# Kernel optimization log

Measured on AMD Instinct MI355X. Metric: run time of the kernel, lower is better.

The kernel has to match this reference:

```python
import jax, jax.numpy as jnp
import numpy as np

U = 128  # linear_units

def setup_inputs() -> dict:
    key = jax.random.key(0)
    k1, k2, k3, k4, k5, k6 = jax.random.split(key, 6)
    B, S, D = 16, 2048, 128
    x = jax.random.normal(k1, (B, S, D), dtype=jnp.float32)
    t = jax.random.uniform(k2, (B, S), dtype=jnp.float32)
    # glorot_uniform inits
    lim_qk = np.sqrt(6.0 / (D + U)).astype(np.float32)
    Wq = jax.random.uniform(k3, (D, U), minval=-lim_qk, maxval=lim_qk, dtype=jnp.float32)
    Wk = jax.random.uniform(k4, (D, U), minval=-lim_qk, maxval=lim_qk, dtype=jnp.float32)
    lim_s = np.sqrt(6.0 / (1 + S)).astype(np.float32)
    theta = jax.random.uniform(k5, (1, S), minval=-lim_s, maxval=lim_s, dtype=jnp.float32)
    mu = jax.random.uniform(k6, (1, S), minval=-lim_s, maxval=lim_s, dtype=jnp.float32)
    return {"x": x, "t": t, "Wq": Wq, "Wk": Wk, "theta": theta, "mu": mu}

def reference(x, t, Wq, Wk, theta, mu):
    # x: (B,S,D), t: (B,S), theta/mu: (1,S)
    scale = jnp.sqrt(jnp.asarray(U, dtype=x.dtype))
    q = x @ Wq                                   # (B,S,U)
    k = x @ Wk                                   # (B,S,U)
    scores = jnp.einsum('biu,bju->bij', q, k) / scale  # (B,S,S)
    alphas = jax.nn.softmax(scores, axis=-1)
    gn = jnp.einsum('bij,bjd->bid', alphas, x)   # weighted sum == alphas @ x, (B,S,D)
    time_fact = jax.nn.sigmoid(theta - mu * t)   # (B,S)
    v = jnp.sum(gn * time_fact[:, :, None], axis=1)  # (B,D)
    return v
```

## Files before the change

### kernel.cpp

```cpp
#include <hip/hip_runtime.h>
#include <hip/hip_bf16.h>

#define SS 2048
#define DD 128
#define BB 16
#define LDST 136
#define SCT 268

typedef short bf16x8 __attribute__((ext_vector_type(8)));
typedef float f32x4 __attribute__((ext_vector_type(4)));
typedef unsigned short ushort_t;

__device__ __forceinline__ unsigned short f2bf(float f) {
  union { float f; unsigned u; } v; v.f = f;
  unsigned r = v.u + 0x7fffu + ((v.u >> 16) & 1u);
  return (unsigned short)(r >> 16);
}
__device__ __forceinline__ float fexp2(float x) { return __builtin_amdgcn_exp2f(x); }


__global__ __launch_bounds__(256) void wprep(
    const float* __restrict__ Wq, const float* __restrict__ Wk,
    ushort_t* __restrict__ wt_g) {
  int idx = blockIdx.x * 256 + threadIdx.x;
  int r = idx & 16383, uu = r >> 7, d = r & 127;
  if (idx < 16384)
    wt_g[uu * 128 + d] = f2bf(Wq[d * 128 + uu] * 0.1275174346f);
  else
    wt_g[(uu + 128) * 128 + d] = f2bf(Wk[d * 128 + uu]);
}

__global__ __launch_bounds__(256, 2) void qk_gemm(
    const float* __restrict__ x, const ushort_t* __restrict__ wt_g,
    uint4* __restrict__ qF, uint4* __restrict__ kF) {
  __shared__ ushort_t xs[64 * LDST];
  __shared__ ushort_t sc[64 * SCT];
  const int tid = threadIdx.x, wave = tid >> 6, lane = tid & 63;
  const int lq = lane & 15, quad = lane >> 4;
  const int m0 = blockIdx.x * 64;

#pragma unroll
  for (int i = 0; i < 8; ++i) {
    int idx = i * 256 + tid;
    int row = idx >> 5, c4 = (idx & 31) * 4;
    const float4 v = *(const float4*)(x + (size_t)(m0 + row) * DD + c4);
    ushort4 h;
    h.x = f2bf(v.x); h.y = f2bf(v.y); h.z = f2bf(v.z); h.w = f2bf(v.w);
    *(ushort4*)(&xs[row * LDST + c4]) = h;
  }
  bf16x8 wf[4][4];
#pragma unroll
  for (int nt = 0; nt < 4; ++nt)
#pragma unroll
    for (int ks = 0; ks < 4; ++ks)
      wf[nt][ks] = *(const bf16x8*)(wt_g + (wave * 64 + nt * 16 + lq) * 128 + ks * 32 + quad * 8);
  __syncthreads();

  f32x4 acc[4][4];
#pragma unroll
  for (int mt = 0; mt < 4; ++mt)
#pragma unroll
    for (int nt = 0; nt < 4; ++nt) acc[mt][nt] = (f32x4){0.f, 0.f, 0.f, 0.f};
#pragma unroll
  for (int mt = 0; mt < 4; ++mt) {
    bf16x8 af[4];
#pragma unroll
    for (int ks = 0; ks < 4; ++ks)
      af[ks] = *(const bf16x8*)(&xs[(mt * 16 + lq) * LDST + ks * 32 + quad * 8]);
#pragma unroll
    for (int nt = 0; nt < 4; ++nt)
#pragma unroll
      for (int ks = 0; ks < 4; ++ks)
        acc[mt][nt] = __builtin_amdgcn_mfma_f32_16x16x32_bf16(af[ks], wf[nt][ks], acc[mt][nt], 0, 0, 0);
  }
#pragma unroll
  for (int mt = 0; mt < 4; ++mt)
#pragma unroll
    for (int nt = 0; nt < 4; ++nt)
#pragma unroll
      for (int r = 0; r < 4; ++r)
        sc[(mt * 16 + quad * 4 + r) * SCT + wave * 64 + nt * 16 + lq] = f2bf(acc[mt][nt][r]);
  __syncthreads();
#pragma unroll
  for (int i = 0; i < 8; ++i) {
    int c = i * 256 + tid;
    int lane_c = c & 63, ks_c = (c >> 6) & 3, g_c = (c >> 8) & 3, isk = c >> 10;
    int li = lane_c & 15, qd = lane_c >> 4;
    int col = isk * 128 + ks_c * 32 + qd * 8;
    uint4 v = *(const uint4*)(&sc[(g_c * 16 + li) * SCT + col]);
    size_t G = (size_t)blockIdx.x * 4 + g_c;
    uint4* dst = isk ? kF : qF;
    dst[(G * 4 + ks_c) * 64 + lane_c] = v;
  }
}

__global__ __launch_bounds__(256, 4) void attn_p1(
    const uint4* __restrict__ qF, const uint4* __restrict__ kF,
    float* __restrict__ l) {
  const int bx = blockIdx.x;
  const int b = bx >> 6, ib = (bx >> 1) & 31, jh = bx & 1;
  const int tid = threadIdx.x, wave = tid >> 6, lane = tid & 63;
  const int lq = lane & 15, quad = lane >> 4;
  __shared__ float rs_lds[4][64];

  const bf16x8* qc = (const bf16x8*)qF;
  bf16x8 af[4][4];
#pragma unroll
  for (int mt = 0; mt < 4; ++mt)
#pragma unroll
    for (int ks = 0; ks < 4; ++ks)
      af[mt][ks] = qc[((size_t)(b * 128 + ib * 4 + mt) * 4 + ks) * 64 + lane];

  const bf16x8* kb = (const bf16x8*)kF + (size_t)b * 128 * 4 * 64 + lane;

  float rowsum[4][4];
#pragma unroll
  for (int mt = 0; mt < 4; ++mt)
#pragma unroll
    for (int r = 0; r < 4; ++r) rowsum[mt][r] = 0.f;

  const f32x4 z4 = {0.f, 0.f, 0.f, 0.f};
  for (int it = 0; it < 16; ++it) {
    int g = jh * 64 + it * 4 + wave;
    bf16x8 f[4];
#pragma unroll
    for (int ks = 0; ks < 4; ++ks) f[ks] = kb[((size_t)g * 4 + ks) * 64];
    f32x4 a[4];
    __builtin_amdgcn_s_setprio(1);
#pragma unroll
    for (int mt = 0; mt < 4; ++mt)
      a[mt] = __builtin_amdgcn_mfma_f32_16x16x32_bf16(af[mt][0], f[0], z4, 0, 0, 0);
#pragma unroll
    for (int ks = 1; ks < 4; ++ks)
#pragma unroll
      for (int mt = 0; mt < 4; ++mt)
        a[mt] = __builtin_amdgcn_mfma_f32_16x16x32_bf16(af[mt][ks], f[ks], a[mt], 0, 0, 0);
    __builtin_amdgcn_s_setprio(0);
#pragma unroll
    for (int mt = 0; mt < 4; ++mt)
#pragma unroll
      for (int r = 0; r < 4; ++r) rowsum[mt][r] += fexp2(a[mt][r]);
  }

#pragma unroll
  for (int d2 = 1; d2 <= 8; d2 <<= 1)
#pragma unroll
    for (int mt = 0; mt < 4; ++mt)
#pragma unroll
      for (int r = 0; r < 4; ++r)
        rowsum[mt][r] += __shfl_xor(rowsum[mt][r], d2, 64);
  if (lq == 0) {
#pragma unroll
    for (int mt = 0; mt < 4; ++mt)
#pragma unroll
      for (int r = 0; r < 4; ++r)
        rs_lds[wave][mt * 16 + quad * 4 + r] = rowsum[mt][r];
  }
  __syncthreads();
  if (tid < 64) {
    float p = rs_lds[0][tid] + rs_lds[1][tid] + rs_lds[2][tid] + rs_lds[3][tid];
    atomicAdd(&l[b * SS + ib * 64 + tid], p);
  }
}

__global__ __launch_bounds__(256, 4) void attn_p2(
    const uint4* __restrict__ qF, const uint4* __restrict__ kF,
    const float* __restrict__ t, const float* __restrict__ theta,
    const float* __restrict__ mu, const float* __restrict__ l,
    float* __restrict__ w) {
  const int bx = blockIdx.x;
  const int b = bx >> 6, ib = (bx >> 1) & 31, jh = bx & 1;
  const int tid = threadIdx.x, wave = tid >> 6, lane = tid & 63;
  const int lq = lane & 15, quad = lane >> 4;
  __shared__ float c_lds[64];

  if (tid < 64) {
    int gi = ib * 64 + tid;
    float z = theta[gi] - mu[gi] * t[b * SS + gi];
    float tf = 1.f / (1.f + fexp2(-z * 1.44269504f));
    c_lds[tid] = tf / l[b * SS + gi];
  }
  __syncthreads();

  const bf16x8* qc = (const bf16x8*)qF;
  bf16x8 af[4][4];
#pragma unroll
  for (int mt = 0; mt < 4; ++mt)
#pragma unroll
    for (int ks = 0; ks < 4; ++ks)
      af[mt][ks] = qc[((size_t)(b * 128 + ib * 4 + mt) * 4 + ks) * 64 + lane];

  float creg[4][4];
#pragma unroll
  for (int mt = 0; mt < 4; ++mt)
#pragma unroll
    for (int r = 0; r < 4; ++r) creg[mt][r] = c_lds[mt * 16 + quad * 4 + r];

  const bf16x8* kb = (const bf16x8*)kF + (size_t)b * 128 * 4 * 64 + lane;
  const f32x4 z4 = {0.f, 0.f, 0.f, 0.f};

  for (int it = 0; it < 16; ++it) {
    int g = jh * 64 + it * 4 + wave;
    bf16x8 f[4];
#pragma unroll
    for (int ks = 0; ks < 4; ++ks) f[ks] = kb[((size_t)g * 4 + ks) * 64];
    f32x4 a[4];
    __builtin_amdgcn_s_setprio(1);
#pragma unroll
    for (int mt = 0; mt < 4; ++mt)
      a[mt] = __builtin_amdgcn_mfma_f32_16x16x32_bf16(af[mt][0], f[0], z4, 0, 0, 0);
#pragma unroll
    for (int ks = 1; ks < 4; ++ks)
#pragma unroll
      for (int mt = 0; mt < 4; ++mt)
        a[mt] = __builtin_amdgcn_mfma_f32_16x16x32_bf16(af[mt][ks], f[ks], a[mt], 0, 0, 0);
    __builtin_amdgcn_s_setprio(0);
    float cs = 0.f;
#pragma unroll
    for (int mt = 0; mt < 4; ++mt)
#pragma unroll
      for (int r = 0; r < 4; ++r) cs = fmaf(creg[mt][r], fexp2(a[mt][r]), cs);
    cs += __shfl_xor(cs, 16, 64);
    cs += __shfl_xor(cs, 32, 64);
    if (lane < 16) atomicAdd(&w[b * SS + g * 16 + lane], cs);
  }
}

__global__ __launch_bounds__(256) void finalize(
    const float* __restrict__ x, const float* __restrict__ w,
    float* __restrict__ out) {
  const int b = blockIdx.x >> 5;
  const int j0 = (blockIdx.x & 31) * 64;
  const int tid = threadIdx.x;
  const int d = tid & 127, jo = tid >> 7;
  float acc = 0.f;
  for (int jj = 0; jj < 32; ++jj) {
    int j = j0 + jj * 2 + jo;
    acc = fmaf(w[b * SS + j], x[((size_t)b * SS + j) * DD + d], acc);
  }
  __shared__ float red[256];
  red[tid] = acc;
  __syncthreads();
  if (tid < 128) atomicAdd(&out[b * DD + tid], red[tid] + red[tid + 128]);
}

extern "C" void kernel_launch(void* const* d_in, const int* in_sizes, int n_in,
                              void* d_out, int out_size, void* d_ws, size_t ws_size,
                              hipStream_t stream) {
  const float* x = (const float*)d_in[0];
  const float* t = (const float*)d_in[1];
  const float* Wq = (const float*)d_in[2];
  const float* Wk = (const float*)d_in[3];
  const float* theta = (const float*)d_in[4];
  const float* mu = (const float*)d_in[5];
  float* out = (float*)d_out;

  uint4* qF = (uint4*)d_ws;
  uint4* kF = qF + (size_t)2048 * 4 * 64;
  ushort_t* wt_g = (ushort_t*)(kF + (size_t)2048 * 4 * 64);
  float* w = (float*)(wt_g + 256 * 128);
  float* l = w + (size_t)BB * SS;

  hipMemsetAsync(w, 0, (size_t)BB * SS * sizeof(float), stream);
  hipMemsetAsync(l, 0, (size_t)BB * SS * sizeof(float), stream);
  hipMemsetAsync(d_out, 0, (size_t)BB * DD * sizeof(float), stream);

  wprep<<<dim3(128), dim3(256), 0, stream>>>(Wq, Wk, wt_g);
  qk_gemm<<<dim3(512), dim3(256), 0, stream>>>(x, wt_g, qF, kF);
  attn_p1<<<dim3(1024), dim3(256), 0, stream>>>(qF, kF, l);
  attn_p2<<<dim3(1024), dim3(256), 0, stream>>>(qF, kF, t, theta, mu, l, w);
  finalize<<<dim3(512), dim3(256), 0, stream>>>(x, w, out);
}
```

Measured before the change: 131.9 us.

## Stage 128-row Q tiles in LDS and swizzle block order across batches

Each attention block now covers 128 query rows (up from 64) against a quarter of the keys, with the Q fragments staged in shared memory rather than held in registers. This halves how often each K fragment is reloaded per query row. Block indices are remapped so neighbouring blocks interleave batches, and each block starts its key loop at a rotated offset to spread L2/HBM traffic. In exchange there is 32KB of LDS per block and an LDS read for every MFMA operand, which may limit occupancy and add LDS bandwidth pressure.

```diff
diff --git a/kernel.cpp b/kernel.cpp
--- a/kernel.cpp
+++ b/kernel.cpp
@@ -94,50 +94,64 @@
   }
 }
 
+__device__ __forceinline__ void attn_decode(int bx, int& b, int& ii, int& jq) {
+  int x = bx & 7, s = bx >> 3;
+  b = x + ((s >> 6) << 3);
+  int r = s & 63;
+  ii = r >> 2;
+  jq = r & 3;
+}
+
 __global__ __launch_bounds__(256, 4) void attn_p1(
     const uint4* __restrict__ qF, const uint4* __restrict__ kF,
     float* __restrict__ l) {
-  const int bx = blockIdx.x;
-  const int b = bx >> 6, ib = (bx >> 1) & 31, jh = bx & 1;
+  int b, ii, jq;
+  attn_decode(blockIdx.x, b, ii, jq);
   const int tid = threadIdx.x, wave = tid >> 6, lane = tid & 63;
   const int lq = lane & 15, quad = lane >> 4;
-  __shared__ float rs_lds[4][64];
-
-  const bf16x8* qc = (const bf16x8*)qF;
-  bf16x8 af[4][4];
-#pragma unroll
-  for (int mt = 0; mt < 4; ++mt)
-#pragma unroll
-    for (int ks = 0; ks < 4; ++ks)
-      af[mt][ks] = qc[((size_t)(b * 128 + ib * 4 + mt) * 4 + ks) * 64 + lane];
-
+  __shared__ uint4 qs[2048];
+  __shared__ float rs_lds[4][128];
+
+  {
+    const uint4* qbase = qF + (size_t)(b * 128 + ii * 8) * 4 * 64;
+#pragma unroll
+    for (int i = 0; i < 8; ++i) qs[i * 256 + tid] = qbase[i * 256 + tid];
+  }
+  __syncthreads();
+
+  const uint4* qsl = qs + lane;
   const bf16x8* kb = (const bf16x8*)kF + (size_t)b * 128 * 4 * 64 + lane;
-
-  float rowsum[4][4];
-#pragma unroll
-  for (int mt = 0; mt < 4; ++mt)
+  const int rot = ii & 7;
+
+  float rowsum[8][4];
+#pragma unroll
+  for (int mt = 0; mt < 8; ++mt)
 #pragma unroll
     for (int r = 0; r < 4; ++r) rowsum[mt][r] = 0.f;
 
   const f32x4 z4 = {0.f, 0.f, 0.f, 0.f};
-  for (int it = 0; it < 16; ++it) {
-    int g = jh * 64 + it * 4 + wave;
+  for (int it = 0; it < 8; ++it) {
+    int g = jq * 32 + (((it + rot) & 7) << 2) + wave;
     bf16x8 f[4];
 #pragma unroll
     for (int ks = 0; ks < 4; ++ks) f[ks] = kb[((size_t)g * 4 + ks) * 64];
-    f32x4 a[4];
+    f32x4 a[8];
     __builtin_amdgcn_s_setprio(1);
 #pragma unroll
-    for (int mt = 0; mt < 4; ++mt)
-      a[mt] = __builtin_amdgcn_mfma_f32_16x16x32_bf16(af[mt][0], f[0], z4, 0, 0, 0);
+    for (int mt = 0; mt < 8; ++mt) {
+      bf16x8 q0 = *(const bf16x8*)(qsl + (mt * 4 + 0) * 64);
+      a[mt] = __builtin_amdgcn_mfma_f32_16x16x32_bf16(q0, f[0], z4, 0, 0, 0);
+    }
 #pragma unroll
     for (int ks = 1; ks < 4; ++ks)
 #pragma unroll
-      for (int mt = 0; mt < 4; ++mt)
-        a[mt] = __builtin_amdgcn_mfma_f32_16x16x32_bf16(af[mt][ks], f[ks], a[mt], 0, 0, 0);
+      for (int mt = 0; mt < 8; ++mt) {
+        bf16x8 qk = *(const bf16x8*)(qsl + (mt * 4 + ks) * 64);
+        a[mt] = __builtin_amdgcn_mfma_f32_16x16x32_bf16(qk, f[ks], a[mt], 0, 0, 0);
+      }
     __builtin_amdgcn_s_setprio(0);
 #pragma unroll
-    for (int mt = 0; mt < 4; ++mt)
+    for (int mt = 0; mt < 8; ++mt)
 #pragma unroll
       for (int r = 0; r < 4; ++r) rowsum[mt][r] += fexp2(a[mt][r]);
   }
@@ -145,21 +159,21 @@
 #pragma unroll
   for (int d2 = 1; d2 <= 8; d2 <<= 1)
 #pragma unroll
-    for (int mt = 0; mt < 4; ++mt)
+    for (int mt = 0; mt < 8; ++mt)
 #pragma unroll
       for (int r = 0; r < 4; ++r)
         rowsum[mt][r] += __shfl_xor(rowsum[mt][r], d2, 64);
   if (lq == 0) {
 #pragma unroll
-    for (int mt = 0; mt < 4; ++mt)
+    for (int mt = 0; mt < 8; ++mt)
 #pragma unroll
       for (int r = 0; r < 4; ++r)
         rs_lds[wave][mt * 16 + quad * 4 + r] = rowsum[mt][r];
   }
   __syncthreads();
-  if (tid < 64) {
+  if (tid < 128) {
     float p = rs_lds[0][tid] + rs_lds[1][tid] + rs_lds[2][tid] + rs_lds[3][tid];
-    atomicAdd(&l[b * SS + ib * 64 + tid], p);
+    atomicAdd(&l[b * SS + ii * 128 + tid], p);
   }
 }
 
@@ -168,56 +182,60 @@
     const float* __restrict__ t, const float* __restrict__ theta,
     const float* __restrict__ mu, const float* __restrict__ l,
     float* __restrict__ w) {
-  const int bx = blockIdx.x;
-  const int b = bx >> 6, ib = (bx >> 1) & 31, jh = bx & 1;
+  int b, ii, jq;
+  attn_decode(blockIdx.x, b, ii, jq);
   const int tid = threadIdx.x, wave = tid >> 6, lane = tid & 63;
   const int lq = lane & 15, quad = lane >> 4;
-  __shared__ float c_lds[64];
-
-  if (tid < 64) {
-    int gi = ib * 64 + tid;
+  __shared__ uint4 qs[2048];
+  __shared__ float c_lds[128];
+
+  {
+    const uint4* qbase = qF + (size_t)(b * 128 + ii * 8) * 4 * 64;
+#pragma unroll
+    for (int i = 0; i < 8; ++i) qs[i * 256 + tid] = qbase[i * 256 + tid];
+  }
+  if (tid < 128) {
+    int gi = ii * 128 + tid;
     float z = theta[gi] - mu[gi] * t[b * SS + gi];
     float tf = 1.f / (1.f + fexp2(-z * 1.44269504f));
     c_lds[tid] = tf / l[b * SS + gi];
   }
   __syncthreads();
 
-  const bf16x8* qc = (const bf16x8*)qF;
-  bf16x8 af[4][4];
-#pragma unroll
-  for (int mt = 0; mt < 4; ++mt)
-#pragma unroll
-    for (int ks = 0; ks < 4; ++ks)
-      af[mt][ks] = qc[((size_t)(b * 128 + ib * 4 + mt) * 4 + ks) * 64 + lane];
-
-  float creg[4][4];
-#pragma unroll
-  for (int mt = 0; mt < 4; ++mt)
+  const uint4* qsl = qs + lane;
+  float creg[8][4];
+#pragma unroll
+  for (int mt = 0; mt < 8; ++mt)
 #pragma unroll
     for (int r = 0; r < 4; ++r) creg[mt][r] = c_lds[mt * 16 + quad * 4 + r];
 
   const bf16x8* kb = (const bf16x8*)kF + (size_t)b * 128 * 4 * 64 + lane;
+  const int rot = ii & 7;
   const f32x4 z4 = {0.f, 0.f, 0.f, 0.f};
 
-  for (int it = 0; it < 16; ++it) {
-    int g = jh * 64 + it * 4 + wave;
+  for (int it = 0; it < 8; ++it) {
+    int g = jq * 32 + (((it + rot) & 7) << 2) + wave;
     bf16x8 f[4];
 #pragma unroll
     for (int ks = 0; ks < 4; ++ks) f[ks] = kb[((size_t)g * 4 + ks) * 64];
-    f32x4 a[4];
+    f32x4 a[8];
     __builtin_amdgcn_s_setprio(1);
 #pragma unroll
-    for (int mt = 0; mt < 4; ++mt)
-      a[mt] = __builtin_amdgcn_mfma_f32_16x16x32_bf16(af[mt][0], f[0], z4, 0, 0, 0);
+    for (int mt = 0; mt < 8; ++mt) {
+      bf16x8 q0 = *(const bf16x8*)(qsl + (mt * 4 + 0) * 64);
+      a[mt] = __builtin_amdgcn_mfma_f32_16x16x32_bf16(q0, f[0], z4, 0, 0, 0);
+    }
 #pragma unroll
     for (int ks = 1; ks < 4; ++ks)
 #pragma unroll
-      for (int mt = 0; mt < 4; ++mt)
-        a[mt] = __builtin_amdgcn_mfma_f32_16x16x32_bf16(af[mt][ks], f[ks], a[mt], 0, 0, 0);
+      for (int mt = 0; mt < 8; ++mt) {
+        bf16x8 qk = *(const bf16x8*)(qsl + (mt * 4 + ks) * 64);
+        a[mt] = __builtin_amdgcn_mfma_f32_16x16x32_bf16(qk, f[ks], a[mt], 0, 0, 0);
+      }
     __builtin_amdgcn_s_setprio(0);
     float cs = 0.f;
 #pragma unroll
-    for (int mt = 0; mt < 4; ++mt)
+    for (int mt = 0; mt < 8; ++mt)
 #pragma unroll
       for (int r = 0; r < 4; ++r) cs = fmaf(creg[mt][r], fexp2(a[mt][r]), cs);
     cs += __shfl_xor(cs, 16, 64);
```

After: 181.8 us. 37.8% more time.

## Stage K tiles through double-buffered LDS shared by waves with larger query tiles

Applied to the files above, without the earlier changes.

The attention passes now give each block 256 query rows (64 per wave) against a quarter of the keys. K fragments are loaded cooperatively into a double-buffered LDS tile and shared by all four waves, where before each wave streamed its own K directly from global memory. Block indices are remapped so neighbouring blocks cover different batches, and the p1 row-sum reduction now uses per-wave atomics. This cuts global K traffic per FLOP but halves the grid and lowers the occupancy hint to 2 blocks per CU. It also adds barriers and 32KB of LDS per block.

```diff
diff --git a/kernel.cpp b/kernel.cpp
--- a/kernel.cpp
+++ b/kernel.cpp
@@ -94,14 +94,22 @@
   }
 }
 
-__global__ __launch_bounds__(256, 4) void attn_p1(
+__device__ __forceinline__ void attn_decode(int bx, int& b, int& ii, int& jq) {
+  int x = bx & 7, s = bx >> 3;
+  b = x + ((s >> 5) << 3);
+  int r = s & 31;
+  ii = r >> 2;
+  jq = r & 3;
+}
+
+__global__ __launch_bounds__(256, 2) void attn_p1(
     const uint4* __restrict__ qF, const uint4* __restrict__ kF,
     float* __restrict__ l) {
-  const int bx = blockIdx.x;
-  const int b = bx >> 6, ib = (bx >> 1) & 31, jh = bx & 1;
+  int b, ii, jq;
+  attn_decode(blockIdx.x, b, ii, jq);
   const int tid = threadIdx.x, wave = tid >> 6, lane = tid & 63;
   const int lq = lane & 15, quad = lane >> 4;
-  __shared__ float rs_lds[4][64];
+  __shared__ uint4 kbuf[2][1024];
 
   const bf16x8* qc = (const bf16x8*)qF;
   bf16x8 af[4][4];
@@ -109,9 +117,18 @@
   for (int mt = 0; mt < 4; ++mt)
 #pragma unroll
     for (int ks = 0; ks < 4; ++ks)
-      af[mt][ks] = qc[((size_t)(b * 128 + ib * 4 + mt) * 4 + ks) * 64 + lane];
-
-  const bf16x8* kb = (const bf16x8*)kF + (size_t)b * 128 * 4 * 64 + lane;
+      af[mt][ks] = qc[((size_t)(b * 128 + ii * 16 + wave * 4 + mt) * 4 + ks) * 64 + lane];
+
+  const uint4* kbase = kF + (size_t)(b * 128 + jq * 32) * 4 * 64;
+  uint4 st_r[4];
+  auto issue_load = [&](int st) {
+#pragma unroll
+    for (int i = 0; i < 4; ++i) st_r[i] = kbase[(size_t)st * 1024 + i * 256 + tid];
+  };
+  auto write_lds = [&](int buf) {
+#pragma unroll
+    for (int i = 0; i < 4; ++i) kbuf[buf][i * 256 + tid] = st_r[i];
+  };
 
   float rowsum[4][4];
 #pragma unroll
@@ -120,26 +137,35 @@
     for (int r = 0; r < 4; ++r) rowsum[mt][r] = 0.f;
 
   const f32x4 z4 = {0.f, 0.f, 0.f, 0.f};
-  for (int it = 0; it < 16; ++it) {
-    int g = jh * 64 + it * 4 + wave;
-    bf16x8 f[4];
-#pragma unroll
-    for (int ks = 0; ks < 4; ++ks) f[ks] = kb[((size_t)g * 4 + ks) * 64];
-    f32x4 a[4];
-    __builtin_amdgcn_s_setprio(1);
-#pragma unroll
-    for (int mt = 0; mt < 4; ++mt)
-      a[mt] = __builtin_amdgcn_mfma_f32_16x16x32_bf16(af[mt][0], f[0], z4, 0, 0, 0);
-#pragma unroll
-    for (int ks = 1; ks < 4; ++ks)
+  issue_load(0);
+  for (int st = 0; st < 8; ++st) {
+    const int cur = st & 1;
+    write_lds(cur);
+    if (st < 7) issue_load(st + 1);
+    __syncthreads();
+#pragma unroll
+    for (int g2 = 0; g2 < 4; ++g2) {
+      bf16x8 f[4];
+#pragma unroll
+      for (int ks = 0; ks < 4; ++ks)
+        f[ks] = *(const bf16x8*)&kbuf[cur][(g2 * 4 + ks) * 64 + lane];
+      f32x4 a[4];
+      __builtin_amdgcn_s_setprio(1);
 #pragma unroll
       for (int mt = 0; mt < 4; ++mt)
-        a[mt] = __builtin_amdgcn_mfma_f32_16x16x32_bf16(af[mt][ks], f[ks], a[mt], 0, 0, 0);
-    __builtin_amdgcn_s_setprio(0);
-#pragma unroll
-    for (int mt = 0; mt < 4; ++mt)
-#pragma unroll
-      for (int r = 0; r < 4; ++r) rowsum[mt][r] += fexp2(a[mt][r]);
+        a[mt] = __builtin_amdgcn_mfma_f32_16x16x32_bf16(af[mt][0], f[0], z4, 0, 0, 0);
+#pragma unroll
+      for (int ks = 1; ks < 4; ++ks)
+#pragma unroll
+        for (int mt = 0; mt < 4; ++mt)
+          a[mt] = __builtin_amdgcn_mfma_f32_16x16x32_bf16(af[mt][ks], f[ks], a[mt], 0, 0, 0);
+      __builtin_amdgcn_s_setprio(0);
+#pragma unroll
+      for (int mt = 0; mt < 4; ++mt)
+#pragma unroll
+        for (int r = 0; r < 4; ++r) rowsum[mt][r] += fexp2(a[mt][r]);
+    }
+    __syncthreads();
   }
 
 #pragma unroll
@@ -154,33 +180,29 @@
     for (int mt = 0; mt < 4; ++mt)
 #pragma unroll
       for (int r = 0; r < 4; ++r)
-        rs_lds[wave][mt * 16 + quad * 4 + r] = rowsum[mt][r];
-  }
-  __syncthreads();
-  if (tid < 64) {
-    float p = rs_lds[0][tid] + rs_lds[1][tid] + rs_lds[2][tid] + rs_lds[3][tid];
-    atomicAdd(&l[b * SS + ib * 64 + tid], p);
-  }
-}
-
-__global__ __launch_bounds__(256, 4) void attn_p2(
+        atomicAdd(&l[b * SS + ii * 256 + (wave * 4 + mt) * 16 + quad * 4 + r],
+                  rowsum[mt][r]);
+  }
+}
+
+__global__ __launch_bounds__(256, 2) void attn_p2(
     const uint4* __restrict__ qF, const uint4* __restrict__ kF,
     const float* __restrict__ t, const float* __restrict__ theta,
     const float* __restrict__ mu, const float* __restrict__ l,
     float* __restrict__ w) {
-  const int bx = blockIdx.x;
-  const int b = bx >> 6, ib = (bx >> 1) & 31, jh = bx & 1;
+  int b, ii, jq;
+  attn_decode(blockIdx.x, b, ii, jq);
   const int tid = threadIdx.x, wave = tid >> 6, lane = tid & 63;
   const int lq = lane & 15, quad = lane >> 4;
-  __shared__ float c_lds[64];
-
-  if (tid < 64) {
-    int gi = ib * 64 + tid;
+  __shared__ uint4 kbuf[2][1024];
+  __shared__ float c_lds[256];
+
+  {
+    int gi = ii * 256 + tid;
     float z = theta[gi] - mu[gi] * t[b * SS + gi];
     float tf = 1.f / (1.f + fexp2(-z * 1.44269504f));
     c_lds[tid] = tf / l[b * SS + gi];
   }
-  __syncthreads();
 
   const bf16x8* qc = (const bf16x8*)qF;
   bf16x8 af[4][4];
@@ -188,41 +210,62 @@
   for (int mt = 0; mt < 4; ++mt)
 #pragma unroll
     for (int ks = 0; ks < 4; ++ks)
-      af[mt][ks] = qc[((size_t)(b * 128 + ib * 4 + mt) * 4 + ks) * 64 + lane];
-
+      af[mt][ks] = qc[((size_t)(b * 128 + ii * 16 + wave * 4 + mt) * 4 + ks) * 64 + lane];
+
+  const uint4* kbase = kF + (size_t)(b * 128 + jq * 32) * 4 * 64;
+  uint4 st_r[4];
+  auto issue_load = [&](int st) {
+#pragma unroll
+    for (int i = 0; i < 4; ++i) st_r[i] = kbase[(size_t)st * 1024 + i * 256 + tid];
+  };
+  auto write_lds = [&](int buf) {
+#pragma unroll
+    for (int i = 0; i < 4; ++i) kbuf[buf][i * 256 + tid] = st_r[i];
+  };
+
+  issue_load(0);
+  __syncthreads();
   float creg[4][4];
 #pragma unroll
   for (int mt = 0; mt < 4; ++mt)
 #pragma unroll
-    for (int r = 0; r < 4; ++r) creg[mt][r] = c_lds[mt * 16 + quad * 4 + r];
-
-  const bf16x8* kb = (const bf16x8*)kF + (size_t)b * 128 * 4 * 64 + lane;
+    for (int r = 0; r < 4; ++r)
+      creg[mt][r] = c_lds[(wave * 4 + mt) * 16 + quad * 4 + r];
+
   const f32x4 z4 = {0.f, 0.f, 0.f, 0.f};
-
-  for (int it = 0; it < 16; ++it) {
-    int g = jh * 64 + it * 4 + wave;
-    bf16x8 f[4];
-#pragma unroll
-    for (int ks = 0; ks < 4; ++ks) f[ks] = kb[((size_t)g * 4 + ks) * 64];
-    f32x4 a[4];
-    __builtin_amdgcn_s_setprio(1);
-#pragma unroll
-    for (int mt = 0; mt < 4; ++mt)
-      a[mt] = __builtin_amdgcn_mfma_f32_16x16x32_bf16(af[mt][0], f[0], z4, 0, 0, 0);
-#pragma unroll
-    for (int ks = 1; ks < 4; ++ks)
+  for (int st = 0; st < 8; ++st) {
+    const int cur = st & 1;
+    write_lds(cur);
+    if (st < 7) issue_load(st + 1);
+    __syncthreads();
+#pragma unroll
+    for (int g2 = 0; g2 < 4; ++g2) {
+      bf16x8 f[4];
+#pragma unroll
+      for (int ks = 0; ks < 4; ++ks)
+        f[ks] = *(const bf16x8*)&kbuf[cur][(g2 * 4 + ks) * 64 + lane];
+      f32x4 a[4];
+      __builtin_amdgcn_s_setprio(1);
 #pragma unroll
       for (int mt = 0; mt < 4; ++mt)
-        a[mt] = __builtin_amdgcn_mfma_f32_16x16x32_bf16(af[mt][ks], f[ks], a[mt], 0, 0, 0);
-    __builtin_amdgcn_s_setprio(0);
-    float cs = 0.f;
-#pragma unroll
-    for (int mt = 0; mt < 4; ++mt)
-#pragma unroll
-      for (int r = 0; r < 4; ++r) cs = fmaf(creg[mt][r], fexp2(a[mt][r]), cs);
-    cs += __shfl_xor(cs, 16, 64);
-    cs += __shfl_xor(cs, 32, 64);
-    if (lane < 16) atomicAdd(&w[b * SS + g * 16 + lane], cs);
+        a[mt] = __builtin_amdgcn_mfma_f32_16x16x32_bf16(af[mt][0], f[0], z4, 0, 0, 0);
+#pragma unroll
+      for (int ks = 1; ks < 4; ++ks)
+#pragma unroll
+        for (int mt = 0; mt < 4; ++mt)
+          a[mt] = __builtin_amdgcn_mfma_f32_16x16x32_bf16(af[mt][ks], f[ks], a[mt], 0, 0, 0);
+      __builtin_amdgcn_s_setprio(0);
+      float cs = 0.f;
+#pragma unroll
+      for (int mt = 0; mt < 4; ++mt)
+#pragma unroll
+        for (int r = 0; r < 4; ++r) cs = fmaf(creg[mt][r], fexp2(a[mt][r]), cs);
+      cs += __shfl_xor(cs, 16, 64);
+      cs += __shfl_xor(cs, 32, 64);
+      if (lane < 16)
+        atomicAdd(&w[b * SS + (jq * 32 + st * 4 + g2) * 16 + lane], cs);
+    }
+    __syncthreads();
   }
 }
 
@@ -267,7 +310,7 @@
 
   wprep<<<dim3(128), dim3(256), 0, stream>>>(Wq, Wk, wt_g);
   qk_gemm<<<dim3(512), dim3(256), 0, stream>>>(x, wt_g, qF, kF);
-  attn_p1<<<dim3(1024), dim3(256), 0, stream>>>(qF, kF, l);
-  attn_p2<<<dim3(1024), dim3(256), 0, stream>>>(qF, kF, t, theta, mu, l, w);
+  attn_p1<<<dim3(512), dim3(256), 0, stream>>>(qF, kF, l);
+  attn_p2<<<dim3(512), dim3(256), 0, stream>>>(qF, kF, t, theta, mu, l, w);
   finalize<<<dim3(512), dim3(256), 0, stream>>>(x, w, out);
 }
```

Measured after the change: 148.1 us. 1.12x slower.
